# Kernel optimization log

Measured on AMD Instinct MI355X. Metric: run time of the kernel, lower is better.

Reference implementation:

```python
import jax, jax.numpy as jnp
import numpy as np

N = 100000
E = 400000
NFEAT, NHID, NOUT, NHEAD = 128, 64, 128, 4
HIDDEN = NHID * NHEAD  # 256
SLOPE = 0.2


def gat_conv(x, src, dst, W, a_src, a_dst, b, concat):
    """PyG-style GATConv (eval mode, self-loops already appended to src/dst).
    x: [N, Fin]; W: [Fin, H*C]; a_src/a_dst: [H, C]; b: [H*C] or [C]."""
    H, C = a_src.shape
    h = (x @ W).reshape(N, H, C)                      # [N,H,C]
    al_s = (h * a_src).sum(-1)                        # [N,H] per-node src score
    al_d = (h * a_dst).sum(-1)                        # [N,H] per-node dst score
    e = jax.nn.leaky_relu(al_s[src] + al_d[dst], SLOPE)  # [Et,H]
    # segment softmax over incoming edges of each dst node
    m = jax.ops.segment_max(e, dst, num_segments=N)
    m = jnp.where(jnp.isfinite(m), m, 0.0)
    ex = jnp.exp(e - m[dst])
    denom = jax.ops.segment_sum(ex, dst, num_segments=N)
    alpha = ex / (denom[dst] + 1e-16)                 # [Et,H]
    msg = alpha[:, :, None] * h[src]                  # [Et,H,C]
    out = jax.ops.segment_sum(msg, dst, num_segments=N)  # [N,H,C]
    out = out.reshape(N, H * C) if concat else out.mean(axis=1)
    return out + b


def setup_inputs() -> dict:
    key = jax.random.key(0)
    ks = jax.random.split(key, 16)
    x = jax.random.normal(ks[0], (N, NFEAT), dtype=jnp.float32)
    edge_index = jax.random.randint(ks[1], (2, E), 0, N, dtype=jnp.int64)
    s = 0.1
    inp = {
        'x': x, 'edge_index': edge_index,
        # layer 0: nfeat -> nhid x nhead (concat)
        'W0': jax.random.normal(ks[2], (NFEAT, HIDDEN), jnp.float32) * s,
        'as0': jax.random.normal(ks[3], (NHEAD, NHID), jnp.float32) * s,
        'ad0': jax.random.normal(ks[4], (NHEAD, NHID), jnp.float32) * s,
        'b0': jnp.zeros((HIDDEN,), jnp.float32),
        # layer 1: hidden -> nhid x nhead (concat)
        'W1': jax.random.normal(ks[5], (HIDDEN, HIDDEN), jnp.float32) * s,
        'as1': jax.random.normal(ks[6], (NHEAD, NHID), jnp.float32) * s,
        'ad1': jax.random.normal(ks[7], (NHEAD, NHID), jnp.float32) * s,
        'b1': jnp.zeros((HIDDEN,), jnp.float32),
        # output layer: hidden -> nout, heads=1, concat=False
        'W2': jax.random.normal(ks[8], (HIDDEN, NOUT), jnp.float32) * s,
        'as2': jax.random.normal(ks[9], (1, NOUT), jnp.float32) * s,
        'ad2': jax.random.normal(ks[10], (1, NOUT), jnp.float32) * s,
        'b2': jnp.zeros((NOUT,), jnp.float32),
    }
    return inp


def reference(x, edge_index, W0, as0, ad0, b0, W1, as1, ad1, b1, W2, as2, ad2, b2):
    # PyG GATConv adds self-loops by default; edge set is shared across layers.
    loop = jnp.arange(N, dtype=edge_index.dtype)
    src = jnp.concatenate([edge_index[0], loop])
    dst = jnp.concatenate([edge_index[1], loop])
    # dropout inactive in eval mode
    h = jax.nn.elu(gat_conv(x, src, dst, W0, as0, ad0, b0, concat=True))
    h = jax.nn.elu(gat_conv(h, src, dst, W1, as1, ad1, b1, concat=True))
    out = gat_conv(h, src, dst, W2, as2, ad2, b2, concat=False)
    return out
```

## Files before the change

### kernel.cpp

```cpp
#include <hip/hip_runtime.h>
#include <cmath>

#define NN 100000
#define EE 400000
#define ET (EE + NN)
#define SLOPE 0.2f

typedef __attribute__((ext_vector_type(8))) short short8;
typedef __attribute__((ext_vector_type(4))) float floatx4;

__device__ __forceinline__ float bl(uint u) {
    union { unsigned int i; float f; } v; v.i = u << 16; return v.f;
}
__device__ __forceinline__ float bh(uint u) {
    union { unsigned int i; float f; } v; v.i = u & 0xffff0000u; return v.f;
}
__device__ __forceinline__ ushort f2b(float f) {
    union { float f; unsigned int i; } v; v.f = f;
    unsigned int r = v.i + 0x7FFFu + ((v.i >> 16) & 1u);
    return (ushort)(r >> 16);
}

__device__ __forceinline__ void gload16(const ushort* g, ushort* l) {
    __builtin_amdgcn_global_load_lds((const __attribute__((address_space(1))) void*)g,
                                     (__attribute__((address_space(3))) void*)l, 16, 0, 0);
}

__global__ __launch_bounds__(256) void count_deg(const int* __restrict__ ei, int* __restrict__ deg) {
    int e = blockIdx.x * 256 + threadIdx.x;
    if (e < EE) atomicAdd(&deg[ei[EE + e]], 1);
}

__global__ __launch_bounds__(256) void scan1(const int* __restrict__ deg, int* __restrict__ incl,
                                             int* __restrict__ bsums) {
    __shared__ int ts[256];
    int b = blockIdx.x, t = threadIdx.x;
    int base = b * 1024 + t * 4;
    int v[4];
#pragma unroll
    for (int i = 0; i < 4; i++) {
        int n = base + i;
        v[i] = (n < NN) ? (deg[n] + 1) : 0;
    }
    int s = 0;
#pragma unroll
    for (int i = 0; i < 4; i++) { s += v[i]; v[i] = s; }
    ts[t] = s;
    __syncthreads();
    for (int off = 1; off < 256; off <<= 1) {
        int x = (t >= off) ? ts[t - off] : 0;
        __syncthreads();
        ts[t] += x;
        __syncthreads();
    }
    int excl = ts[t] - s;
#pragma unroll
    for (int i = 0; i < 4; i++) {
        int n = base + i;
        if (n < NN) incl[n] = v[i] + excl;
    }
    if (t == 255) bsums[b] = ts[255];
}

__global__ __launch_bounds__(128) void scan2(int* __restrict__ bsums, int nblk) {
    __shared__ int ts[128];
    int t = threadIdx.x;
    int v = (t < nblk) ? bsums[t] : 0;
    ts[t] = v;
    __syncthreads();
    for (int off = 1; off < 128; off <<= 1) {
        int x = (t >= off) ? ts[t - off] : 0;
        __syncthreads();
        ts[t] += x;
        __syncthreads();
    }
    if (t < nblk) bsums[t] = ts[t] - v;
}

__global__ __launch_bounds__(256) void scan3(const int* __restrict__ incl, const int* __restrict__ deg,
                                             const int* __restrict__ bsums, int* __restrict__ row_ptr,
                                             int* __restrict__ cursor) {
    int n = blockIdx.x * 256 + threadIdx.x;
    if (n < NN) {
        int rp = incl[n] - (deg[n] + 1) + bsums[n >> 10];
        row_ptr[n] = rp;
        cursor[n] = rp;
    }
    if (n == 0) row_ptr[NN] = ET;
}

__global__ __launch_bounds__(256) void scatter(const int* __restrict__ ei, int* __restrict__ cursor,
                                               int* __restrict__ col) {
    int e = blockIdx.x * 256 + threadIdx.x;
    if (e < EE) {
        int d = ei[EE + e];
        int p = atomicAdd(&cursor[d], 1);
        col[p] = ei[e];
    }
}

__global__ __launch_bounds__(256) void selfloop(const int* __restrict__ cursor, int* __restrict__ col) {
    int n = blockIdx.x * 256 + threadIdx.x;
    if (n < NN) col[cursor[n]] = n;
}

__global__ __launch_bounds__(256) void cast_to_bf16(const float* __restrict__ in,
                                                    ushort* __restrict__ out, int n4) {
    int i = blockIdx.x * 256 + threadIdx.x;
    if (i < n4) {
        float4 v = ((const float4*)in)[i];
        ushort4 o;
        o.x = f2b(v.x); o.y = f2b(v.y); o.z = f2b(v.z); o.w = f2b(v.w);
        ((ushort4*)out)[i] = o;
    }
}

__global__ __launch_bounds__(256) void transpose_cast_all(const float* __restrict__ W0,
                                                          const float* __restrict__ W1,
                                                          const float* __restrict__ W2,
                                                          ushort* __restrict__ Wt0,
                                                          ushort* __restrict__ Wt1,
                                                          ushort* __restrict__ Wt2) {
    int idx = blockIdx.x * 256 + threadIdx.x;
    if (idx < 32768) {
        int n = idx >> 7, k = idx & 127;
        Wt0[idx] = f2b(W0[(size_t)k * 256 + n]);
    } else if (idx < 32768 + 65536) {
        int j = idx - 32768;
        int n = j >> 8, k = j & 255;
        Wt1[j] = f2b(W1[(size_t)k * 256 + n]);
    } else if (idx < 131072) {
        int j = idx - 98304;
        int n = j >> 8, k = j & 255;
        Wt2[j] = f2b(W2[(size_t)k * 128 + n]);
    }
}

__global__ __launch_bounds__(256) void gemm_bf16(const ushort* __restrict__ A,
                                                 const ushort* __restrict__ Bt,
                                                 ushort* __restrict__ C,
                                                 int M, int K, int N,
                                                 const float* __restrict__ asf,
                                                 const float* __restrict__ adf,
                                                 float* __restrict__ als,
                                                 float* __restrict__ ald,
                                                 int H, int lgC) {
    __shared__ __attribute__((aligned(16))) ushort As[128 * 64];
    __shared__ __attribute__((aligned(16))) ushort Bs[128 * 64];
    int tid = threadIdx.x;
    int bm = blockIdx.x * 128;
    int bn = blockIdx.y * 128;
    int wave = tid >> 6, lane = tid & 63;
    int wm = (wave >> 1) * 64, wn = (wave & 1) * 64;

    floatx4 acc[4][4];
#pragma unroll
    for (int i = 0; i < 4; i++)
#pragma unroll
        for (int j = 0; j < 4; j++) acc[i][j] = (floatx4)0.f;

    int rsub = lane >> 3;
    int klog8 = ((lane & 7) ^ rsub) * 8;
    const ushort* aS = A + (size_t)(bm + wave * 8 + rsub) * K + klog8;
    const ushort* bS = Bt + (size_t)(bn + wave * 8 + rsub) * K + klog8;
    ushort* ldsA = &As[wave * 512];
    ushort* ldsB = &Bs[wave * 512];

    int frow = lane & 15;
    int q = lane >> 4;
    int f7 = frow & 7;

    for (int k0 = 0; k0 < K; k0 += 64) {
#pragma unroll
        for (int i = 0; i < 4; i++) {
            gload16(aS + (size_t)i * 32 * K + k0, ldsA + i * 2048);
            gload16(bS + (size_t)i * 32 * K + k0, ldsB + i * 2048);
        }
        __syncthreads();

#pragma unroll
        for (int kk = 0; kk < 2; kk++) {
            short8 afr[4], bfr[4];
            int phys = ((kk * 4 + q) ^ f7) * 8;
#pragma unroll
            for (int i = 0; i < 4; i++)
                afr[i] = *(const short8*)&As[(wm + i * 16 + frow) * 64 + phys];
#pragma unroll
            for (int j = 0; j < 4; j++)
                bfr[j] = *(const short8*)&Bs[(wn + j * 16 + frow) * 64 + phys];
#pragma unroll
            for (int i = 0; i < 4; i++)
#pragma unroll
                for (int j = 0; j < 4; j++)
                    acc[i][j] = __builtin_amdgcn_mfma_f32_16x16x32_bf16(afr[i], bfr[j], acc[i][j], 0, 0, 0);
        }
        __syncthreads();
    }

    int ccol = bn + wn + (lane & 15);
    int crow = bm + wm + (lane >> 4) * 4;
#pragma unroll
    for (int i = 0; i < 4; i++) {
#pragma unroll
        for (int reg = 0; reg < 4; reg++) {
            int row = crow + i * 16 + reg;
            if (row < M) {
#pragma unroll
                for (int j = 0; j < 4; j++)
                    C[(size_t)row * N + ccol + j * 16] = f2b(acc[i][j][reg]);
            }
        }
    }

    {
        int cb = bn + wn + (lane & 15);
        float asv[4], adv[4];
#pragma unroll
        for (int j = 0; j < 4; j++) {
            asv[j] = asf[cb + j * 16];
            adv[j] = adf[cb + j * 16];
        }
        int hidx = (bn + wn) >> lgC;
#pragma unroll
        for (int i = 0; i < 4; i++) {
#pragma unroll
            for (int reg = 0; reg < 4; reg++) {
                float ss = acc[i][0][reg] * asv[0] + acc[i][1][reg] * asv[1]
                         + acc[i][2][reg] * asv[2] + acc[i][3][reg] * asv[3];
                float dd = acc[i][0][reg] * adv[0] + acc[i][1][reg] * adv[1]
                         + acc[i][2][reg] * adv[2] + acc[i][3][reg] * adv[3];
#pragma unroll
                for (int off = 1; off < 16; off <<= 1) {
                    ss += __shfl_xor(ss, off, 64);
                    dd += __shfl_xor(dd, off, 64);
                }
                int row = crow + i * 16 + reg;
                if ((lane & 15) == 0 && row < M) {
                    if (lgC == 6) {
                        als[row * H + hidx] = ss;
                        ald[row * H + hidx] = dd;
                    } else {
                        atomicAdd(&als[row], ss);
                        atomicAdd(&ald[row], dd);
                    }
                }
            }
        }
    }
}

template <int NU, int HC>
__device__ __forceinline__ void gather8(const int* sA, const float* wA,
                                        const ushort* __restrict__ hlin, uint hl, float* acc) {
    if constexpr (NU == 4) {
        uint4 U[8];
#pragma unroll
        for (int d = 0; d < 8; d++)
            U[d] = *((const uint4*)(hlin + (size_t)sA[d] * HC) + hl);
#pragma unroll
        for (int d = 0; d < 8; d++) {
            float w = wA[d];
            acc[0] += w * bl(U[d].x); acc[1] += w * bh(U[d].x);
            acc[2] += w * bl(U[d].y); acc[3] += w * bh(U[d].y);
            acc[4] += w * bl(U[d].z); acc[5] += w * bh(U[d].z);
            acc[6] += w * bl(U[d].w); acc[7] += w * bh(U[d].w);
        }
    } else {
        uint2 U[8];
#pragma unroll
        for (int d = 0; d < 8; d++)
            U[d] = *((const uint2*)(hlin + (size_t)sA[d] * HC) + hl);
#pragma unroll
        for (int d = 0; d < 8; d++) {
            float w = wA[d];
            acc[0] += w * bl(U[d].x); acc[1] += w * bh(U[d].x);
            acc[2] += w * bl(U[d].y); acc[3] += w * bh(U[d].y);
        }
    }
}

template <int H, int HC, bool ELU_ACT, bool OUT_BF16>
__global__ __launch_bounds__(256) void aggregate2(const ushort* __restrict__ hlin,
                                                  const float* __restrict__ als,
                                                  const float* __restrict__ ald,
                                                  const int* __restrict__ row_ptr,
                                                  const int* __restrict__ col,
                                                  const float* __restrict__ bias,
                                                  void* __restrict__ outv) {
    constexpr int CP = HC / 32;
    constexpr int GS = 32 / H;
    constexpr int NU = CP / 2;
    int wv = threadIdx.x >> 6, lane = threadIdx.x & 63;
    int hl = lane & 31;
    int dst = blockIdx.x * 8 + wv * 2 + (lane >> 5);
    int rs = row_ptr[dst];
    int deg = row_ptr[dst + 1] - rs;
    int eg = hl & (GS - 1);
    int head = hl / GS;
    float ad = ald[dst * H + head];

    float acc[CP];
#pragma unroll
    for (int j = 0; j < CP; j++) acc[j] = 0.f;

    int degB = __shfl_xor(deg, 32, 64);

    if (deg <= GS) {
        int src = 0;
        float s = -1e30f;
        if (eg < deg) {
            src = col[rs + eg];
            float sc = als[src * H + head] + ad;
            s = sc > 0.f ? sc : SLOPE * sc;
        }
        float m = s;
#pragma unroll
        for (int off = 1; off < GS; off <<= 1) m = fmaxf(m, __shfl_xor(m, off, 64));
        float e = (eg < deg) ? __expf(s - m) : 0.f;
        float sum = e;
#pragma unroll
        for (int off = 1; off < GS; off <<= 1) sum += __shfl_xor(sum, off, 64);
        float w = e * (1.0f / (sum + 1e-16f));

        int sbase = lane & 32;
        int wbase = (lane & 32) | (hl & ~(GS - 1));

        if constexpr (GS == 8) {
            int sA[8]; float wA[8];
#pragma unroll
            for (int d = 0; d < 8; d++) {
                sA[d] = __shfl(src, sbase + d, 64);
                wA[d] = __shfl(w, wbase + d, 64);
            }
            gather8<NU, HC>(sA, wA, hlin, hl, acc);
        } else {
            int mdeg = max(deg, (degB <= GS) ? degB : 0);
            for (int d0 = 0; d0 < mdeg; d0 += 8) {
                int sA[8]; float wA[8];
#pragma unroll
                for (int d = 0; d < 8; d++) {
                    sA[d] = __shfl(src, sbase + d0 + d, 64);
                    wA[d] = __shfl(w, wbase + d0 + d, 64);
                }
                gather8<NU, HC>(sA, wA, hlin, hl, acc);
            }
        }
    } else {
        float m = -1e30f;
        for (int e2 = eg; e2 < deg; e2 += GS) {
            int s0 = col[rs + e2];
            float sc = als[s0 * H + head] + ad;
            sc = sc > 0.f ? sc : SLOPE * sc;
            m = fmaxf(m, sc);
        }
#pragma unroll
        for (int off = 1; off < GS; off <<= 1) m = fmaxf(m, __shfl_xor(m, off, 64));
        float sum = 0.f;
        for (int e2 = eg; e2 < deg; e2 += GS) {
            int s0 = col[rs + e2];
            float sc = als[s0 * H + head] + ad;
            sc = sc > 0.f ? sc : SLOPE * sc;
            sum += __expf(sc - m);
        }
#pragma unroll
        for (int off = 1; off < GS; off <<= 1) sum += __shfl_xor(sum, off, 64);
        float inv = 1.0f / (sum + 1e-16f);
        for (int d = 0; d < deg; d++) {
            int sd = col[rs + d];
            float sc = als[sd * H + head] + ad;
            sc = sc > 0.f ? sc : SLOPE * sc;
            float wd = __expf(sc - m) * inv;
            const uint* p = (const uint*)(hlin + (size_t)sd * HC) + hl * NU;
#pragma unroll
            for (int qq = 0; qq < NU; qq++) {
                uint u = p[qq];
                acc[2*qq]   += wd * bl(u);
                acc[2*qq+1] += wd * bh(u);
            }
        }
    }

#pragma unroll
    for (int j = 0; j < CP; j++) {
        float v = acc[j] + bias[hl * CP + j];
        if (ELU_ACT) v = v > 0.f ? v : (__expf(v) - 1.0f);
        acc[j] = v;
    }
    if (OUT_BF16) {
        uint* outp = (uint*)((ushort*)outv + (size_t)dst * HC) + hl * NU;
        uint pk[NU];
#pragma unroll
        for (int qq = 0; qq < NU; qq++)
            pk[qq] = (uint)f2b(acc[2*qq]) | ((uint)f2b(acc[2*qq+1]) << 16);
#pragma unroll
        for (int qq = 0; qq < NU; qq++) outp[qq] = pk[qq];
    } else {
        float* outp = (float*)outv + (size_t)dst * HC + hl * CP;
#pragma unroll
        for (int j = 0; j < CP; j++) outp[j] = acc[j];
    }
}

extern "C" void kernel_launch(void* const* d_in, const int* in_sizes, int n_in,
                              void* d_out, int out_size, void* d_ws, size_t ws_size,
                              hipStream_t stream) {
    const float* x   = (const float*)d_in[0];
    const int*   ei  = (const int*)d_in[1];
    const float* W0  = (const float*)d_in[2];
    const float* as0 = (const float*)d_in[3];
    const float* ad0 = (const float*)d_in[4];
    const float* b0  = (const float*)d_in[5];
    const float* W1  = (const float*)d_in[6];
    const float* as1 = (const float*)d_in[7];
    const float* ad1 = (const float*)d_in[8];
    const float* b1  = (const float*)d_in[9];
    const float* W2  = (const float*)d_in[10];
    const float* as2 = (const float*)d_in[11];
    const float* ad2 = (const float*)d_in[12];
    const float* b2  = (const float*)d_in[13];
    float* out = (float*)d_out;

    char* ws = (char*)d_ws;
    size_t off = 0;
    auto alloc = [&](size_t bytes) {
        void* p = ws + off;
        off += (bytes + 255) & ~(size_t)255;
        return p;
    };
    ushort* xb   = (ushort*)alloc((size_t)(NN + 128) * 128 * 2);
    ushort* h    = (ushort*)alloc((size_t)NN * 256 * 2);
    ushort* actB = (ushort*)alloc((size_t)(NN + 128) * 256 * 2);
    ushort* actC = (ushort*)alloc((size_t)(NN + 128) * 256 * 2);
    ushort* Wt0  = (ushort*)alloc((size_t)256 * 128 * 2);
    ushort* Wt1  = (ushort*)alloc((size_t)256 * 256 * 2);
    ushort* Wt2  = (ushort*)alloc((size_t)128 * 256 * 2);
    float* als   = (float*)alloc((size_t)NN * 4 * 4);
    float* ald   = (float*)alloc((size_t)NN * 4 * 4);
    float* als2  = (float*)alloc((size_t)NN * 4);
    float* ald2  = (float*)alloc((size_t)NN * 4);
    int* deg     = (int*)alloc((size_t)NN * 4);
    int* incl    = (int*)alloc((size_t)NN * 4);
    int* row_ptr = (int*)alloc((size_t)(NN + 1) * 4);
    int* cursor  = (int*)alloc((size_t)NN * 4);
    int* col     = (int*)alloc((size_t)ET * 4);
    int* bsums   = (int*)alloc(128 * 4);

    const int NBLK = (NN + 1023) / 1024;

    hipMemsetAsync(deg, 0, (size_t)NN * 4, stream);
    hipMemsetAsync(als2, 0, (size_t)NN * 4, stream);
    hipMemsetAsync(ald2, 0, (size_t)NN * 4, stream);
    count_deg<<<(EE + 255) / 256, 256, 0, stream>>>(ei, deg);
    scan1<<<NBLK, 256, 0, stream>>>(deg, incl, bsums);
    scan2<<<1, 128, 0, stream>>>(bsums, NBLK);
    scan3<<<(NN + 255) / 256, 256, 0, stream>>>(incl, deg, bsums, row_ptr, cursor);
    scatter<<<(EE + 255) / 256, 256, 0, stream>>>(ei, cursor, col);
    selfloop<<<(NN + 255) / 256, 256, 0, stream>>>(cursor, col);

    cast_to_bf16<<<(NN * 128 / 4 + 255) / 256, 256, 0, stream>>>(x, xb, NN * 128 / 4);
    transpose_cast_all<<<(131072 + 255) / 256, 256, 0, stream>>>(W0, W1, W2, Wt0, Wt1, Wt2);

    const int GM = (NN + 127) / 128;
    const int NB8 = NN / 8;

    gemm_bf16<<<dim3(GM, 2), 256, 0, stream>>>(xb, Wt0, h, NN, 128, 256, as0, ad0, als, ald, 4, 6);
    aggregate2<4, 256, true, true><<<NB8, 256, 0, stream>>>(h, als, ald, row_ptr, col, b0, actB);

    gemm_bf16<<<dim3(GM, 2), 256, 0, stream>>>(actB, Wt1, h, NN, 256, 256, as1, ad1, als, ald, 4, 6);
    aggregate2<4, 256, true, true><<<NB8, 256, 0, stream>>>(h, als, ald, row_ptr, col, b1, actC);

    gemm_bf16<<<dim3(GM, 1), 256, 0, stream>>>(actC, Wt2, h, NN, 256, 128, as2, ad2, als2, ald2, 1, 7);
    aggregate2<1, 128, false, false><<<NB8, 256, 0, stream>>>(h, als2, ald2, row_ptr, col, b2, out);
}
```

Before: 444.2 us.

## Fuse prep kernels, convert x inside GEMM, swizzle GEMM grid, rework aggregation mapping

Several independent changes. Memsets and the weight transpose are merged into one prep kernel. The scan2 pass is folded into scan3. The fp32-to-bf16 cast of x now happens inside the first GEMM's A-tile load, which removes the xb buffer. The GEMM grid is remapped so the two N-tiles of the same M-rows run adjacently for L2 reuse. Aggregation goes back to one destination per wave with a 4-edge unrolled gather instead of two destinations per wave with an 8-edge batch; this may lower gather parallelism per wave.

```diff
diff --git a/kernel.cpp b/kernel.cpp
--- a/kernel.cpp
+++ b/kernel.cpp
@@ -9,11 +9,8 @@
 typedef __attribute__((ext_vector_type(8))) short short8;
 typedef __attribute__((ext_vector_type(4))) float floatx4;
 
-__device__ __forceinline__ float bl(uint u) {
-    union { unsigned int i; float f; } v; v.i = u << 16; return v.f;
-}
-__device__ __forceinline__ float bh(uint u) {
-    union { unsigned int i; float f; } v; v.i = u & 0xffff0000u; return v.f;
+__device__ __forceinline__ float b2f(ushort u) {
+    union { unsigned int i; float f; } v; v.i = ((unsigned int)u) << 16; return v.f;
 }
 __device__ __forceinline__ ushort f2b(float f) {
     union { float f; unsigned int i; } v; v.f = f;
@@ -24,6 +21,36 @@
 __device__ __forceinline__ void gload16(const ushort* g, ushort* l) {
     __builtin_amdgcn_global_load_lds((const __attribute__((address_space(1))) void*)g,
                                      (__attribute__((address_space(3))) void*)l, 16, 0, 0);
+}
+
+__global__ __launch_bounds__(256) void prep(int* __restrict__ deg,
+                                            float* __restrict__ als2, float* __restrict__ ald2,
+                                            const float* __restrict__ W0, const float* __restrict__ W1,
+                                            const float* __restrict__ W2,
+                                            ushort* __restrict__ Wt0, ushort* __restrict__ Wt1,
+                                            ushort* __restrict__ Wt2) {
+    int idx = blockIdx.x * 256 + threadIdx.x;
+    if (idx < 25000) {
+        ((int4*)deg)[idx] = make_int4(0, 0, 0, 0);
+    } else if (idx < 50000) {
+        ((float4*)als2)[idx - 25000] = make_float4(0.f, 0.f, 0.f, 0.f);
+    } else if (idx < 75000) {
+        ((float4*)ald2)[idx - 50000] = make_float4(0.f, 0.f, 0.f, 0.f);
+    } else {
+        int j = idx - 75000;
+        if (j < 32768) {
+            int n = j >> 7, k = j & 127;
+            Wt0[j] = f2b(W0[(size_t)k * 256 + n]);
+        } else if (j < 98304) {
+            int t = j - 32768;
+            int n = t >> 8, k = t & 255;
+            Wt1[t] = f2b(W1[(size_t)k * 256 + n]);
+        } else if (j < 131072) {
+            int t = j - 98304;
+            int n = t >> 8, k = t & 255;
+            Wt2[t] = f2b(W2[(size_t)k * 128 + n]);
+        }
+    }
 }
 
 __global__ __launch_bounds__(256) void count_deg(const int* __restrict__ ei, int* __restrict__ deg) {
@@ -62,27 +89,25 @@
     if (t == 255) bsums[b] = ts[255];
 }
 
-__global__ __launch_bounds__(128) void scan2(int* __restrict__ bsums, int nblk) {
+__global__ __launch_bounds__(256) void scan3(const int* __restrict__ incl, const int* __restrict__ deg,
+                                             const int* __restrict__ bsums, int* __restrict__ row_ptr,
+                                             int* __restrict__ cursor, int nblk) {
     __shared__ int ts[128];
     int t = threadIdx.x;
-    int v = (t < nblk) ? bsums[t] : 0;
-    ts[t] = v;
+    if (t < 128) ts[t] = (t < nblk) ? bsums[t] : 0;
     __syncthreads();
     for (int off = 1; off < 128; off <<= 1) {
-        int x = (t >= off) ? ts[t - off] : 0;
-        __syncthreads();
-        ts[t] += x;
-        __syncthreads();
-    }
-    if (t < nblk) bsums[t] = ts[t] - v;
-}
-
-__global__ __launch_bounds__(256) void scan3(const int* __restrict__ incl, const int* __restrict__ deg,
-                                             const int* __restrict__ bsums, int* __restrict__ row_ptr,
-                                             int* __restrict__ cursor) {
-    int n = blockIdx.x * 256 + threadIdx.x;
+        int x = 0;
+        if (t < 128 && t >= off) x = ts[t - off];
+        __syncthreads();
+        if (t < 128) ts[t] += x;
+        __syncthreads();
+    }
+    int n = blockIdx.x * 256 + t;
     if (n < NN) {
-        int rp = incl[n] - (deg[n] + 1) + bsums[n >> 10];
+        int b = n >> 10;
+        int base = b ? ts[b - 1] : 0;
+        int rp = incl[n] - (deg[n] + 1) + base;
         row_ptr[n] = rp;
         cursor[n] = rp;
     }
@@ -104,42 +129,11 @@
     if (n < NN) col[cursor[n]] = n;
 }
 
-__global__ __launch_bounds__(256) void cast_to_bf16(const float* __restrict__ in,
-                                                    ushort* __restrict__ out, int n4) {
-    int i = blockIdx.x * 256 + threadIdx.x;
-    if (i < n4) {
-        float4 v = ((const float4*)in)[i];
-        ushort4 o;
-        o.x = f2b(v.x); o.y = f2b(v.y); o.z = f2b(v.z); o.w = f2b(v.w);
-        ((ushort4*)out)[i] = o;
-    }
-}
-
-__global__ __launch_bounds__(256) void transpose_cast_all(const float* __restrict__ W0,
-                                                          const float* __restrict__ W1,
-                                                          const float* __restrict__ W2,
-                                                          ushort* __restrict__ Wt0,
-                                                          ushort* __restrict__ Wt1,
-                                                          ushort* __restrict__ Wt2) {
-    int idx = blockIdx.x * 256 + threadIdx.x;
-    if (idx < 32768) {
-        int n = idx >> 7, k = idx & 127;
-        Wt0[idx] = f2b(W0[(size_t)k * 256 + n]);
-    } else if (idx < 32768 + 65536) {
-        int j = idx - 32768;
-        int n = j >> 8, k = j & 255;
-        Wt1[j] = f2b(W1[(size_t)k * 256 + n]);
-    } else if (idx < 131072) {
-        int j = idx - 98304;
-        int n = j >> 8, k = j & 255;
-        Wt2[j] = f2b(W2[(size_t)k * 128 + n]);
-    }
-}
-
-__global__ __launch_bounds__(256) void gemm_bf16(const ushort* __restrict__ A,
+template <bool CVT>
+__global__ __launch_bounds__(256) void gemm_bf16(const void* __restrict__ Avoid,
                                                  const ushort* __restrict__ Bt,
                                                  ushort* __restrict__ C,
-                                                 int M, int K, int N,
+                                                 int M, int K, int N, int paired,
                                                  const float* __restrict__ asf,
                                                  const float* __restrict__ adf,
                                                  float* __restrict__ als,
@@ -148,8 +142,17 @@
     __shared__ __attribute__((aligned(16))) ushort As[128 * 64];
     __shared__ __attribute__((aligned(16))) ushort Bs[128 * 64];
     int tid = threadIdx.x;
-    int bm = blockIdx.x * 128;
-    int bn = blockIdx.y * 128;
+    int GMc = (M + 127) >> 7;
+    int bmi, bni;
+    if (paired) {
+        int g = blockIdx.x >> 4, ii = blockIdx.x & 15;
+        bmi = g * 8 + (ii & 7);
+        bni = ii >> 3;
+        if (bmi >= GMc) return;
+    } else {
+        bmi = blockIdx.x; bni = 0;
+    }
+    int bm = bmi * 128, bn = bni * 128;
     int wave = tid >> 6, lane = tid & 63;
     int wm = (wave >> 1) * 64, wn = (wave & 1) * 64;
 
@@ -161,20 +164,41 @@
 
     int rsub = lane >> 3;
     int klog8 = ((lane & 7) ^ rsub) * 8;
-    const ushort* aS = A + (size_t)(bm + wave * 8 + rsub) * K + klog8;
-    const ushort* bS = Bt + (size_t)(bn + wave * 8 + rsub) * K + klog8;
     ushort* ldsA = &As[wave * 512];
     ushort* ldsB = &Bs[wave * 512];
+    const ushort* bS = Bt + (size_t)(bn + wave * 8 + rsub) * K + klog8;
+    const ushort* aS = nullptr;
+    if (!CVT) aS = (const ushort*)Avoid + (size_t)(bm + wave * 8 + rsub) * K + klog8;
 
     int frow = lane & 15;
     int q = lane >> 4;
     int f7 = frow & 7;
 
     for (int k0 = 0; k0 < K; k0 += 64) {
-#pragma unroll
-        for (int i = 0; i < 4; i++) {
-            gload16(aS + (size_t)i * 32 * K + k0, ldsA + i * 2048);
-            gload16(bS + (size_t)i * 32 * K + k0, ldsB + i * 2048);
+        if constexpr (CVT) {
+            const float* Af = (const float*)Avoid;
+#pragma unroll
+            for (int i = 0; i < 4; i++) {
+                int arow = bm + wave * 8 + i * 32 + rsub;
+                float4 f0 = make_float4(0.f, 0.f, 0.f, 0.f), f1 = f0;
+                if (arow < M) {
+                    const float4* ap = (const float4*)(Af + (size_t)arow * K + k0 + klog8);
+                    f0 = ap[0]; f1 = ap[1];
+                }
+                uint4 pk;
+                pk.x = (uint)f2b(f0.x) | ((uint)f2b(f0.y) << 16);
+                pk.y = (uint)f2b(f0.z) | ((uint)f2b(f0.w) << 16);
+                pk.z = (uint)f2b(f1.x) | ((uint)f2b(f1.y) << 16);
+                pk.w = (uint)f2b(f1.z) | ((uint)f2b(f1.w) << 16);
+                *(uint4*)&ldsA[i * 2048 + lane * 8] = pk;
+                gload16(bS + (size_t)i * 32 * K + k0, ldsB + i * 2048);
+            }
+        } else {
+#pragma unroll
+            for (int i = 0; i < 4; i++) {
+                gload16(aS + (size_t)i * 32 * K + k0, ldsA + i * 2048);
+                gload16(bS + (size_t)i * 32 * K + k0, ldsB + i * 2048);
+            }
         }
         __syncthreads();
 
@@ -249,61 +273,30 @@
     }
 }
 
-template <int NU, int HC>
-__device__ __forceinline__ void gather8(const int* sA, const float* wA,
-                                        const ushort* __restrict__ hlin, uint hl, float* acc) {
-    if constexpr (NU == 4) {
-        uint4 U[8];
-#pragma unroll
-        for (int d = 0; d < 8; d++)
-            U[d] = *((const uint4*)(hlin + (size_t)sA[d] * HC) + hl);
-#pragma unroll
-        for (int d = 0; d < 8; d++) {
-            float w = wA[d];
-            acc[0] += w * bl(U[d].x); acc[1] += w * bh(U[d].x);
-            acc[2] += w * bl(U[d].y); acc[3] += w * bh(U[d].y);
-            acc[4] += w * bl(U[d].z); acc[5] += w * bh(U[d].z);
-            acc[6] += w * bl(U[d].w); acc[7] += w * bh(U[d].w);
-        }
-    } else {
-        uint2 U[8];
-#pragma unroll
-        for (int d = 0; d < 8; d++)
-            U[d] = *((const uint2*)(hlin + (size_t)sA[d] * HC) + hl);
-#pragma unroll
-        for (int d = 0; d < 8; d++) {
-            float w = wA[d];
-            acc[0] += w * bl(U[d].x); acc[1] += w * bh(U[d].x);
-            acc[2] += w * bl(U[d].y); acc[3] += w * bh(U[d].y);
-        }
-    }
-}
-
 template <int H, int HC, bool ELU_ACT, bool OUT_BF16>
-__global__ __launch_bounds__(256) void aggregate2(const ushort* __restrict__ hlin,
-                                                  const float* __restrict__ als,
-                                                  const float* __restrict__ ald,
-                                                  const int* __restrict__ row_ptr,
-                                                  const int* __restrict__ col,
-                                                  const float* __restrict__ bias,
-                                                  void* __restrict__ outv) {
-    constexpr int CP = HC / 32;
-    constexpr int GS = 32 / H;
-    constexpr int NU = CP / 2;
+__global__ __launch_bounds__(256) void aggregate(const ushort* __restrict__ hlin,
+                                                 const float* __restrict__ als,
+                                                 const float* __restrict__ ald,
+                                                 const int* __restrict__ row_ptr,
+                                                 const int* __restrict__ col,
+                                                 const float* __restrict__ bias,
+                                                 void* __restrict__ outv) {
+    constexpr int CP = HC / 64;
+    constexpr int GS = 64 / H;
     int wv = threadIdx.x >> 6, lane = threadIdx.x & 63;
-    int hl = lane & 31;
-    int dst = blockIdx.x * 8 + wv * 2 + (lane >> 5);
-    int rs = row_ptr[dst];
-    int deg = row_ptr[dst + 1] - rs;
-    int eg = hl & (GS - 1);
-    int head = hl / GS;
+    int dst = blockIdx.x * 4 + wv;
+    if (dst >= NN) return;
+    int rs = row_ptr[dst], re = row_ptr[dst + 1];
+    int deg = re - rs;
+    int eg = lane & (GS - 1);
+    int head = lane / GS;
     float ad = ald[dst * H + head];
 
     float acc[CP];
 #pragma unroll
     for (int j = 0; j < CP; j++) acc[j] = 0.f;
 
-    int degB = __shfl_xor(deg, 32, 64);
+    uint laneoff = (uint)(lane * CP);
 
     if (deg <= GS) {
         int src = 0;
@@ -322,34 +315,44 @@
         for (int off = 1; off < GS; off <<= 1) sum += __shfl_xor(sum, off, 64);
         float w = e * (1.0f / (sum + 1e-16f));
 
-        int sbase = lane & 32;
-        int wbase = (lane & 32) | (hl & ~(GS - 1));
-
-        if constexpr (GS == 8) {
-            int sA[8]; float wA[8];
-#pragma unroll
-            for (int d = 0; d < 8; d++) {
-                sA[d] = __shfl(src, sbase + d, 64);
-                wA[d] = __shfl(w, wbase + d, 64);
-            }
-            gather8<NU, HC>(sA, wA, hlin, hl, acc);
-        } else {
-            int mdeg = max(deg, (degB <= GS) ? degB : 0);
-            for (int d0 = 0; d0 < mdeg; d0 += 8) {
-                int sA[8]; float wA[8];
-#pragma unroll
-                for (int d = 0; d < 8; d++) {
-                    sA[d] = __shfl(src, sbase + d0 + d, 64);
-                    wA[d] = __shfl(w, wbase + d0 + d, 64);
-                }
-                gather8<NU, HC>(sA, wA, hlin, hl, acc);
+        int hbase = head * GS;
+        int d = 0;
+        for (; d + 4 <= deg; d += 4) {
+            int s0 = __shfl(src, d, 64),     s1 = __shfl(src, d + 1, 64);
+            int s2 = __shfl(src, d + 2, 64), s3 = __shfl(src, d + 3, 64);
+            float w0 = __shfl(w, hbase + d, 64),     w1 = __shfl(w, hbase + d + 1, 64);
+            float w2 = __shfl(w, hbase + d + 2, 64), w3 = __shfl(w, hbase + d + 3, 64);
+            const uint* p0 = (const uint*)(hlin + (uint)s0 * HC + laneoff);
+            const uint* p1 = (const uint*)(hlin + (uint)s1 * HC + laneoff);
+            const uint* p2 = (const uint*)(hlin + (uint)s2 * HC + laneoff);
+            const uint* p3 = (const uint*)(hlin + (uint)s3 * HC + laneoff);
+            uint u0[CP / 2], u1[CP / 2], u2[CP / 2], u3[CP / 2];
+#pragma unroll
+            for (int qq = 0; qq < CP / 2; qq++) { u0[qq] = p0[qq]; u1[qq] = p1[qq]; u2[qq] = p2[qq]; u3[qq] = p3[qq]; }
+#pragma unroll
+            for (int qq = 0; qq < CP / 2; qq++) {
+                acc[2*qq]   += w0 * b2f((ushort)(u0[qq] & 0xffff)) + w1 * b2f((ushort)(u1[qq] & 0xffff))
+                             + w2 * b2f((ushort)(u2[qq] & 0xffff)) + w3 * b2f((ushort)(u3[qq] & 0xffff));
+                acc[2*qq+1] += w0 * b2f((ushort)(u0[qq] >> 16)) + w1 * b2f((ushort)(u1[qq] >> 16))
+                             + w2 * b2f((ushort)(u2[qq] >> 16)) + w3 * b2f((ushort)(u3[qq] >> 16));
+            }
+        }
+        for (; d < deg; d++) {
+            int sd = __shfl(src, d, 64);
+            float wd = __shfl(w, hbase + d, 64);
+            const uint* p = (const uint*)(hlin + (uint)sd * HC + laneoff);
+#pragma unroll
+            for (int qq = 0; qq < CP / 2; qq++) {
+                uint u = p[qq];
+                acc[2*qq]   += wd * b2f((ushort)(u & 0xffff));
+                acc[2*qq+1] += wd * b2f((ushort)(u >> 16));
             }
         }
     } else {
         float m = -1e30f;
         for (int e2 = eg; e2 < deg; e2 += GS) {
-            int s0 = col[rs + e2];
-            float sc = als[s0 * H + head] + ad;
+            int sc0 = col[rs + e2];
+            float sc = als[sc0 * H + head] + ad;
             sc = sc > 0.f ? sc : SLOPE * sc;
             m = fmaxf(m, sc);
         }
@@ -357,8 +360,8 @@
         for (int off = 1; off < GS; off <<= 1) m = fmaxf(m, __shfl_xor(m, off, 64));
         float sum = 0.f;
         for (int e2 = eg; e2 < deg; e2 += GS) {
-            int s0 = col[rs + e2];
-            float sc = als[s0 * H + head] + ad;
+            int sc0 = col[rs + e2];
+            float sc = als[sc0 * H + head] + ad;
             sc = sc > 0.f ? sc : SLOPE * sc;
             sum += __expf(sc - m);
         }
@@ -370,32 +373,32 @@
             float sc = als[sd * H + head] + ad;
             sc = sc > 0.f ? sc : SLOPE * sc;
             float wd = __expf(sc - m) * inv;
-            const uint* p = (const uint*)(hlin + (size_t)sd * HC) + hl * NU;
-#pragma unroll
-            for (int qq = 0; qq < NU; qq++) {
+            const uint* p = (const uint*)(hlin + (uint)sd * HC + laneoff);
+#pragma unroll
+            for (int qq = 0; qq < CP / 2; qq++) {
                 uint u = p[qq];
-                acc[2*qq]   += wd * bl(u);
-                acc[2*qq+1] += wd * bh(u);
+                acc[2*qq]   += wd * b2f((ushort)(u & 0xffff));
+                acc[2*qq+1] += wd * b2f((ushort)(u >> 16));
             }
         }
     }
 
 #pragma unroll
     for (int j = 0; j < CP; j++) {
-        float v = acc[j] + bias[hl * CP + j];
+        float v = acc[j] + bias[lane * CP + j];
         if (ELU_ACT) v = v > 0.f ? v : (__expf(v) - 1.0f);
         acc[j] = v;
     }
     if (OUT_BF16) {
-        uint* outp = (uint*)((ushort*)outv + (size_t)dst * HC) + hl * NU;
-        uint pk[NU];
-#pragma unroll
-        for (int qq = 0; qq < NU; qq++)
+        ushort* outp = (ushort*)outv + (size_t)dst * HC + laneoff;
+        uint pk[CP / 2];
+#pragma unroll
+        for (int qq = 0; qq < CP / 2; qq++)
             pk[qq] = (uint)f2b(acc[2*qq]) | ((uint)f2b(acc[2*qq+1]) << 16);
 #pragma unroll
-        for (int qq = 0; qq < NU; qq++) outp[qq] = pk[qq];
+        for (int qq = 0; qq < CP / 2; qq++) ((uint*)outp)[qq] = pk[qq];
     } else {
-        float* outp = (float*)outv + (size_t)dst * HC + hl * CP;
+        float* outp = (float*)outv + (size_t)dst * HC + laneoff;
 #pragma unroll
         for (int j = 0; j < CP; j++) outp[j] = acc[j];
     }
@@ -427,7 +430,6 @@
         off += (bytes + 255) & ~(size_t)255;
         return p;
     };
-    ushort* xb   = (ushort*)alloc((size_t)(NN + 128) * 128 * 2);
     ushort* h    = (ushort*)alloc((size_t)NN * 256 * 2);
     ushort* actB = (ushort*)alloc((size_t)(NN + 128) * 256 * 2);
     ushort* actC = (ushort*)alloc((size_t)(NN + 128) * 256 * 2);
@@ -447,28 +449,24 @@
 
     const int NBLK = (NN + 1023) / 1024;
 
-    hipMemsetAsync(deg, 0, (size_t)NN * 4, stream);
-    hipMemsetAsync(als2, 0, (size_t)NN * 4, stream);
-    hipMemsetAsync(ald2, 0, (size_t)NN * 4, stream);
+    prep<<<(75000 + 131072 + 255) / 256, 256, 0, stream>>>(deg, als2, ald2, W0, W1, W2, Wt0, Wt1, Wt2);
+
     count_deg<<<(EE + 255) / 256, 256, 0, stream>>>(ei, deg);
     scan1<<<NBLK, 256, 0, stream>>>(deg, incl, bsums);
-    scan2<<<1, 128, 0, stream>>>(bsums, NBLK);
-    scan3<<<(NN + 255) / 256, 256, 0, stream>>>(incl, deg, bsums, row_ptr, cursor);
+    scan3<<<(NN + 255) / 256, 256, 0, stream>>>(incl, deg, bsums, row_ptr, cursor, NBLK);
     scatter<<<(EE + 255) / 256, 256, 0, stream>>>(ei, cursor, col);
     selfloop<<<(NN + 255) / 256, 256, 0, stream>>>(cursor, col);
 
-    cast_to_bf16<<<(NN * 128 / 4 + 255) / 256, 256, 0, stream>>>(x, xb, NN * 128 / 4);
-    transpose_cast_all<<<(131072 + 255) / 256, 256, 0, stream>>>(W0, W1, W2, Wt0, Wt1, Wt2);
-
-    const int GM = (NN + 127) / 128;
-    const int NB8 = NN / 8;
-
-    gemm_bf16<<<dim3(GM, 2), 256, 0, stream>>>(xb, Wt0, h, NN, 128, 256, as0, ad0, als, ald, 4, 6);
-    aggregate2<4, 256, true, true><<<NB8, 256, 0, stream>>>(h, als, ald, row_ptr, col, b0, actB);
-
-    gemm_bf16<<<dim3(GM, 2), 256, 0, stream>>>(actB, Wt1, h, NN, 256, 256, as1, ad1, als, ald, 4, 6);
-    aggregate2<4, 256, true, true><<<NB8, 256, 0, stream>>>(h, als, ald, row_ptr, col, b1, actC);
-
-    gemm_bf16<<<dim3(GM, 1), 256, 0, stream>>>(actC, Wt2, h, NN, 256, 128, as2, ad2, als2, ald2, 1, 7);
-    aggregate2<1, 128, false, false><<<NB8, 256, 0, stream>>>(h, als2, ald2, row_ptr, col, b2, out);
-}
+    const int GMc = (NN + 127) / 128;
+    const int GPAIR = 16 * ((GMc + 7) / 8);
+    const int NB4 = (NN + 3) / 4;
+
+    gemm_bf16<true><<<GPAIR, 256, 0, stream>>>(x, Wt0, h, NN, 128, 256, 1, as0, ad0, als, ald, 4, 6);
+    aggregate<4, 256, true, true><<<NB4, 256, 0, stream>>>(h, als, ald, row_ptr, col, b0, actB);
+
+    gemm_bf16<false><<<GPAIR, 256, 0, stream>>>(actB, Wt1, h, NN, 256, 256, 1, as1, ad1, als, ald, 4, 6);
+    aggregate<4, 256, true, true><<<NB4, 256, 0, stream>>>(h, als, ald, row_ptr, col, b1, actC);
+
+    gemm_bf16<false><<<GMc, 256, 0, stream>>>(actC, Wt2, h, NN, 256, 128, 0, as2, ad2, als2, ald2, 1, 7);
+    aggregate<1, 128, false, false><<<NB4, 256, 0, stream>>>(h, als2, ald2, row_ptr, col, b2, out);
+}
```

New measurement: 435.0 us. 2.1% less time.
